# Performance work log

Measured on AMD Instinct MI355X. Metric: run time of the kernel, lower is better.

The kernel has to match this reference:

```python
import jax, jax.numpy as jnp
import numpy as np

B, S, D_MODEL, D_K, D_V, H = 2, 2048, 1024, 1024, 1024, 16


def setup_inputs() -> dict:
    key = jax.random.key(0)
    ks = jax.random.split(key, 12)
    s = 0.02
    inp = {
        "queries": jax.random.normal(ks[0], (B, S, D_MODEL), jnp.float32),
        "keys": jax.random.normal(ks[1], (B, S, D_MODEL), jnp.float32),
        "values": jax.random.normal(ks[2], (B, S, D_MODEL), jnp.float32),
        # causal mask: 1 where attention is disallowed (added as -1e9*mask)
        "mask": jnp.triu(jnp.ones((1, 1, S, S), jnp.float32), k=1),
        "Wq": jax.random.normal(ks[3], (D_MODEL, D_K), jnp.float32) * s,
        "bq": jnp.zeros((D_K,), jnp.float32),
        "Wk": jax.random.normal(ks[4], (D_MODEL, D_K), jnp.float32) * s,
        "bk": jnp.zeros((D_K,), jnp.float32),
        "Wv": jax.random.normal(ks[5], (D_MODEL, D_V), jnp.float32) * s,
        "bv": jnp.zeros((D_V,), jnp.float32),
        "Wo": jax.random.normal(ks[6], (D_K, D_MODEL), jnp.float32) * s,
        "bo": jnp.zeros((D_MODEL,), jnp.float32),
    }
    return inp


def _split_heads(x):  # [B,S,D] -> [B,H,S,D/H]
    b, s, d = x.shape
    return x.reshape(b, s, H, d // H).transpose(0, 2, 1, 3)


def reference(queries, keys, values, mask, Wq, bq, Wk, bk, Wv, bv, Wo, bo):
    q = _split_heads(queries @ Wq + bq)   # [B,H,S,hd]
    k = _split_heads(keys @ Wk + bk)
    v = _split_heads(values @ Wv + bv)
    # NOTE: original scales by sqrt(full d_k), not per-head dim (faithful quirk)
    scores = jnp.einsum("bhqd,bhkd->bhqk", q, k) / jnp.sqrt(jnp.float32(D_K))
    scores = scores + (-1e9) * mask
    w = jax.nn.softmax(scores, axis=-1)
    out = jnp.einsum("bhqk,bhkd->bhqd", w, v)        # [B,H,S,hd]
    out = out.transpose(0, 2, 1, 3).reshape(q.shape[0], q.shape[2], D_K)
    return out @ Wo + bo
```

## Files before the change

### kernel.cpp

```cpp
#include <hip/hip_runtime.h>
#include <hip/hip_bf16.h>
#include <cstdint>

typedef __bf16 bf16;
typedef __bf16 bf16x2 __attribute__((ext_vector_type(2)));
typedef __bf16 bf16x4 __attribute__((ext_vector_type(4)));
typedef __bf16 bf16x8 __attribute__((ext_vector_type(8)));
typedef float f32x4 __attribute__((ext_vector_type(4)));
typedef float f32x16 __attribute__((ext_vector_type(16)));
typedef unsigned int u32;

#define B_ 2
#define S_ 2048
#define DM 1024
#define H_ 16
#define HD 64

__device__ __forceinline__ void gload_lds16(const bf16* g, bf16* l) {
  __builtin_amdgcn_global_load_lds((const __attribute__((address_space(1))) void*)g,
                                   (__attribute__((address_space(3))) void*)l,
                                   16, 0, 0);
}

__device__ __forceinline__ u32 cvt_pk_bf16(float lo, float hi) {
  u32 r;
  asm("v_cvt_pk_bf16_f32 %0, %1, %2" : "=v"(r) : "v"(lo), "v"(hi));
  return r;
}

__global__ __launch_bounds__(256) void convert_k(const float* __restrict__ s0,
                                                 const float* __restrict__ s1,
                                                 const float* __restrict__ s2,
                                                 bf16* __restrict__ d0,
                                                 bf16* __restrict__ d1,
                                                 bf16* __restrict__ d2) {
  const float* s = (blockIdx.z == 0) ? s0 : (blockIdx.z == 1) ? s1 : s2;
  bf16* d = (blockIdx.z == 0) ? d0 : (blockIdx.z == 1) ? d1 : d2;
  const size_t i = ((size_t)blockIdx.x * 256 + threadIdx.x) * 8;
  f32x4 a = *(const f32x4*)(s + i);
  f32x4 b = *(const f32x4*)(s + i + 4);
  bf16x8 o;
#pragma unroll
  for (int j = 0; j < 4; j++) { o[j] = (bf16)a[j]; o[j + 4] = (bf16)b[j]; }
  *(bf16x8*)(d + i) = o;
}

__global__ __launch_bounds__(256) void transposeW_k(
    const float* __restrict__ w0, const float* __restrict__ w1,
    const float* __restrict__ w2, const float* __restrict__ w3,
    bf16* __restrict__ t0, bf16* __restrict__ t1,
    bf16* __restrict__ t2, bf16* __restrict__ t3) {
  const float* src = (blockIdx.z == 0) ? w0 : (blockIdx.z == 1) ? w1
                     : (blockIdx.z == 2) ? w2 : w3;
  bf16* dst = (blockIdx.z == 0) ? t0 : (blockIdx.z == 1) ? t1
              : (blockIdx.z == 2) ? t2 : t3;
  __shared__ float tile[32][33];
  const int tx = threadIdx.x, ty = threadIdx.y;
  const int x0 = blockIdx.x * 32, y0 = blockIdx.y * 32;
#pragma unroll
  for (int r = 0; r < 4; r++)
    tile[ty + r * 8][tx] = src[(size_t)(y0 + ty + r * 8) * DM + x0 + tx];
  __syncthreads();
#pragma unroll
  for (int r = 0; r < 4; r++)
    dst[(size_t)(x0 + ty + r * 8) * DM + y0 + tx] = (bf16)tile[tx][ty + r * 8];
}

struct GArgs { const void* A; const bf16* Bt; const float* bias; void* C; };
struct GArgs3 { GArgs g[3]; };

template <bool AF32, bool CF32>
__global__ __launch_bounds__(256) void gemm_k(GArgs3 args, int M, int N, int K) {
  const GArgs ga = args.g[blockIdx.z];
  __shared__ __align__(16) bf16 As[128 * 32];
  __shared__ __align__(16) bf16 Bs[128 * 32];
  const int tid = threadIdx.x;
  const int lane = tid & 63, w = tid >> 6;
  const int l15 = lane & 15, q = lane >> 4;
  const int wr = w >> 1, wc = w & 1;
  const int m0 = blockIdx.y * 128, n0 = blockIdx.x * 128;

  const int c0 = w * 128 + lane;
  const int c1 = c0 + 64;
  const int r0 = c0 >> 2, r1 = c1 >> 2, koff = (c0 & 3) * 8;
  const bf16* gB0 = ga.Bt + (size_t)(n0 + r0) * K + koff;
  const bf16* gB1 = ga.Bt + (size_t)(n0 + r1) * K + koff;
  bf16* lA0 = As + (w * 2 + 0) * 512;
  bf16* lA1 = As + (w * 2 + 1) * 512;
  bf16* lB0 = Bs + (w * 2 + 0) * 512;
  bf16* lB1 = Bs + (w * 2 + 1) * 512;

  const float* pA0 = nullptr;
  const float* pA1 = nullptr;
  f32x4 t00, t01, t10, t11;
  if constexpr (AF32) {
    const float* A = (const float*)ga.A;
    pA0 = A + (size_t)(m0 + r0) * K + koff;
    pA1 = A + (size_t)(m0 + r1) * K + koff;
    t00 = *(const f32x4*)pA0; t01 = *(const f32x4*)(pA0 + 4);
    t10 = *(const f32x4*)pA1; t11 = *(const f32x4*)(pA1 + 4);
  }

  f32x4 acc[4][4] = {};

  for (int k0 = 0; k0 < K; k0 += 32) {
    if constexpr (AF32) {
      bf16x8 va0, va1;
#pragma unroll
      for (int j = 0; j < 4; j++) {
        va0[j] = (bf16)t00[j]; va0[j + 4] = (bf16)t01[j];
        va1[j] = (bf16)t10[j]; va1[j + 4] = (bf16)t11[j];
      }
      *(bf16x8*)(lA0 + lane * 8) = va0;
      *(bf16x8*)(lA1 + lane * 8) = va1;
    } else {
      const bf16* A = (const bf16*)ga.A;
      gload_lds16(A + (size_t)(m0 + r0) * K + koff + k0, lA0);
      gload_lds16(A + (size_t)(m0 + r1) * K + koff + k0, lA1);
    }
    gload_lds16(gB0 + k0, lB0);
    gload_lds16(gB1 + k0, lB1);
    __syncthreads();

    bf16x8 a[4], b[4];
#pragma unroll
    for (int mt = 0; mt < 4; mt++)
      a[mt] = *(const bf16x8*)(As + (wr * 64 + mt * 16 + l15) * 32 + q * 8);
#pragma unroll
    for (int nt = 0; nt < 4; nt++)
      b[nt] = *(const bf16x8*)(Bs + (wc * 64 + nt * 16 + l15) * 32 + q * 8);

    if constexpr (AF32) {
      const int kn = (k0 + 32 < K) ? k0 + 32 : k0;
      t00 = *(const f32x4*)(pA0 + kn); t01 = *(const f32x4*)(pA0 + kn + 4);
      t10 = *(const f32x4*)(pA1 + kn); t11 = *(const f32x4*)(pA1 + kn + 4);
    }

#pragma unroll
    for (int mt = 0; mt < 4; mt++)
#pragma unroll
      for (int nt = 0; nt < 4; nt++)
        acc[mt][nt] = __builtin_amdgcn_mfma_f32_16x16x32_bf16(a[mt], b[nt],
                                                              acc[mt][nt], 0, 0, 0);
    __syncthreads();
  }

#pragma unroll
  for (int nt = 0; nt < 4; nt++) {
    const int col = n0 + wc * 64 + nt * 16 + l15;
    const float bv = ga.bias[col];
#pragma unroll
    for (int mt = 0; mt < 4; mt++) {
      const int row = m0 + wr * 64 + mt * 16 + q * 4;
#pragma unroll
      for (int r = 0; r < 4; r++) {
        const float val = acc[mt][nt][r] + bv;
        if constexpr (CF32)
          ((float*)ga.C)[(size_t)(row + r) * N + col] = val;
        else
          ((bf16*)ga.C)[(size_t)(row + r) * N + col] = (bf16)val;
      }
    }
  }
}

__global__ __launch_bounds__(256, 4) void attn_k(const bf16* __restrict__ Qp,
                                                 const bf16* __restrict__ Kp,
                                                 const bf16* __restrict__ Vp,
                                                 bf16* __restrict__ Op) {
  const int g = blockIdx.x;
  const int c = g & 255, sl = g >> 8;
  const int u = c & 31;
  const int xt = (sl == 0) ? u : (sl == 1) ? 31 - u
                 : (sl == 2) ? (u ^ 16) : 31 - (u ^ 16);
  const int h = (c >> 5) | ((sl & 1) << 3);
  const int b = sl >> 1;
  const int i0 = xt * 64;

  const int tid = threadIdx.x;
  const int lane = tid & 63, w = tid >> 6;
  const int l31 = lane & 31, hi = lane >> 5;
  const int qh = w >> 1, kh = w & 1;

  __shared__ __align__(16) char smem[36864];
  bf16 (*Ks)[64][72] = (bf16 (*)[64][72])smem;
  bf16 (*Vts)[64][72] = (bf16 (*)[64][72])(smem + 18432);

  const size_t headoff = (size_t)b * S_ * DM + h * HD;
  const bf16* Kb = Kp + headoff;
  const bf16* Vb = Vp + headoff;

  const int kr0 = tid >> 3, kr1 = 32 + (tid >> 3), kcb = (tid & 7) * 8;
  const int d0 = (tid & 31) * 2, kq = (tid >> 5) * 8;
  const float QSCALE = 0.04508422f;

  bf16x8 qreg[4];
  {
    const bf16* qb = Qp + headoff + (size_t)(i0 + qh * 32 + l31) * DM + hi * 8;
#pragma unroll
    for (int kk = 0; kk < 4; kk++) {
      bf16x8 v = *(const bf16x8*)(qb + kk * 16);
      bf16x8 o;
#pragma unroll
      for (int j = 0; j < 8; j++) o[j] = (bf16)((float)v[j] * QSCALE);
      qreg[kk] = o;
    }
  }

  {
    bf16x8 k0v = *(const bf16x8*)(Kb + (size_t)kr0 * DM + kcb);
    bf16x8 k1v = *(const bf16x8*)(Kb + (size_t)kr1 * DM + kcb);
    *(bf16x8*)&Ks[0][kr0][kcb] = k0v;
    *(bf16x8*)&Ks[0][kr1][kcb] = k1v;
    bf16x8 vlo, vhi;
#pragma unroll
    for (int j = 0; j < 8; j++) {
      bf16x2 p = *(const bf16x2*)(Vb + (size_t)(kq + j) * DM + d0);
      vlo[j] = p[0]; vhi[j] = p[1];
    }
    *(bf16x8*)&Vts[0][d0][kq] = vlo;
    *(bf16x8*)&Vts[0][d0 + 1][kq] = vhi;
  }
  __syncthreads();

  f32x16 oacc0 = {}, oacc1 = {};
  float rsum = 0.f;
  int buf = 0;

  for (int j0 = 0; j0 <= i0; j0 += 64, buf ^= 1) {
    const int jn = (j0 + 64 <= i0) ? j0 + 64 : 0;
    bf16x8 kpre0 = *(const bf16x8*)(Kb + (size_t)(jn + kr0) * DM + kcb);
    bf16x8 kpre1 = *(const bf16x8*)(Kb + (size_t)(jn + kr1) * DM + kcb);
    bf16x2 vpre[8];
#pragma unroll
    for (int j = 0; j < 8; j++)
      vpre[j] = *(const bf16x2*)(Vb + (size_t)(jn + kq + j) * DM + d0);

    const bool diag = (j0 == i0);
    if (!(diag && kh > qh)) {
      f32x16 sacc = {};
      __builtin_amdgcn_s_setprio(1);
#pragma unroll
      for (int kk = 0; kk < 4; kk++) {
        bf16x8 ka = *(const bf16x8*)&Ks[buf][kh * 32 + l31][kk * 16 + hi * 8];
        sacc = __builtin_amdgcn_mfma_f32_32x32x16_bf16(ka, qreg[kk], sacc, 0, 0, 0);
      }
      __builtin_amdgcn_s_setprio(0);

      float p[16];
      if (diag) {
        const int qrl = qh * 32 + l31;
#pragma unroll
        for (int r = 0; r < 16; r++) {
          const int keyl = kh * 32 + (r & 3) + 8 * (r >> 2) + 4 * hi;
          p[r] = (keyl <= qrl) ? __builtin_amdgcn_exp2f(sacc[r]) : 0.f;
          rsum += p[r];
        }
      } else {
#pragma unroll
        for (int r = 0; r < 16; r++) {
          p[r] = __builtin_amdgcn_exp2f(sacc[r]);
          rsum += p[r];
        }
      }

      u32 Aq[4][2];
#pragma unroll
      for (int t = 0; t < 4; t++) {
        Aq[t][0] = cvt_pk_bf16(p[4 * t + 0], p[4 * t + 1]);
        Aq[t][1] = cvt_pk_bf16(p[4 * t + 2], p[4 * t + 3]);
      }
      bf16x8 pb[2];
#pragma unroll
      for (int s = 0; s < 2; s++) {
        auto e0 = __builtin_amdgcn_permlane32_swap(Aq[2 * s][0], Aq[2 * s + 1][0], false, false);
        auto e1 = __builtin_amdgcn_permlane32_swap(Aq[2 * s][1], Aq[2 * s + 1][1], false, false);
        union { u32 u[4]; bf16x8 v; } cv;
        cv.u[0] = e0[0]; cv.u[1] = e1[0]; cv.u[2] = e0[1]; cv.u[3] = e1[1];
        pb[s] = cv.v;
      }

      __builtin_amdgcn_s_setprio(1);
#pragma unroll
      for (int s = 0; s < 2; s++) {
        bf16x8 va0 = *(const bf16x8*)&Vts[buf][l31][kh * 32 + s * 16 + hi * 8];
        bf16x8 va1 = *(const bf16x8*)&Vts[buf][32 + l31][kh * 32 + s * 16 + hi * 8];
        oacc0 = __builtin_amdgcn_mfma_f32_32x32x16_bf16(va0, pb[s], oacc0, 0, 0, 0);
        oacc1 = __builtin_amdgcn_mfma_f32_32x32x16_bf16(va1, pb[s], oacc1, 0, 0, 0);
      }
      __builtin_amdgcn_s_setprio(0);
    }

    *(bf16x8*)&Ks[buf ^ 1][kr0][kcb] = kpre0;
    *(bf16x8*)&Ks[buf ^ 1][kr1][kcb] = kpre1;
    {
      bf16x8 vlo, vhi;
#pragma unroll
      for (int j = 0; j < 8; j++) { vlo[j] = vpre[j][0]; vhi[j] = vpre[j][1]; }
      *(bf16x8*)&Vts[buf ^ 1][d0][kq] = vlo;
      *(bf16x8*)&Vts[buf ^ 1][d0 + 1][kq] = vhi;
    }
    __syncthreads();
  }

  float rtot_w = rsum + __shfl_xor(rsum, 32);
  float* osum = (float*)smem;
  float* auxf = (float*)(smem + 32768);
#pragma unroll
  for (int m = 0; m < 2; m++) {
#pragma unroll
    for (int rq = 0; rq < 4; rq++) {
      f32x4 v4;
#pragma unroll
      for (int e = 0; e < 4; e++)
        v4[e] = m ? oacc1[rq * 4 + e] : oacc0[rq * 4 + e];
      *(f32x4*)(osum + w * 2048 + (m * 4 + rq) * 256 + lane * 4) = v4;
    }
  }
  if (lane < 32) auxf[w * 32 + lane] = rtot_w;
  __syncthreads();

  {
    const int q = tid >> 2, q31b = q & 31, qh2 = q >> 5;
    const float rtot = auxf[(qh2 * 2 + 0) * 32 + q31b] + auxf[(qh2 * 2 + 1) * 32 + q31b];
    const float rinv = 1.0f / rtot;
    const int dbase = (tid & 3) * 16;
    bf16* orow = Op + headoff + (size_t)(i0 + q) * DM + dbase;
#pragma unroll
    for (int gg = 0; gg < 2; gg++) {
      bf16x8 o8;
#pragma unroll
      for (int e = 0; e < 8; e++) {
        const int d = dbase + gg * 8 + e;
        const int base = (((d >> 5) << 2) | ((d >> 3) & 3)) * 256 +
                         (q31b + 32 * ((d >> 2) & 1)) * 4 + (d & 3);
        const float v = osum[(qh2 * 2 + 0) * 2048 + base] +
                        osum[(qh2 * 2 + 1) * 2048 + base];
        o8[e] = (bf16)(v * rinv);
      }
      *(bf16x8*)(orow + gg * 8) = o8;
    }
  }
}

extern "C" void kernel_launch(void* const* d_in, const int* in_sizes, int n_in,
                              void* d_out, int out_size, void* d_ws, size_t ws_size,
                              hipStream_t stream) {
  const float* q_in = (const float*)d_in[0];
  const float* k_in = (const float*)d_in[1];
  const float* v_in = (const float*)d_in[2];
  const float* Wq = (const float*)d_in[4];
  const float* bq = (const float*)d_in[5];
  const float* Wk = (const float*)d_in[6];
  const float* bk = (const float*)d_in[7];
  const float* Wv = (const float*)d_in[8];
  const float* bv = (const float*)d_in[9];
  const float* Wo = (const float*)d_in[10];
  const float* bo = (const float*)d_in[11];

  bf16* ws = (bf16*)d_ws;
  const size_t NQ = (size_t)B_ * S_ * DM;
  bf16* Qp = ws;
  bf16* Kp = ws + NQ;
  bf16* Vp = ws + 2 * NQ;
  bf16* WqT = ws + 3 * NQ;
  bf16* WkT = WqT + (size_t)DM * DM;
  bf16* WvT = WkT + (size_t)DM * DM;
  bf16* WoT = WvT + (size_t)DM * DM;
  bf16* qb = WoT + (size_t)DM * DM;
  bf16* kb = qb + NQ;
  bf16* vb = kb + NQ;

  const bool fast = ws_size >= (size_t)(28 * 1024 * 1024) * 2;

  transposeW_k<<<dim3(32, 32, 4), dim3(32, 8), 0, stream>>>(
      Wq, Wk, Wv, Wo, WqT, WkT, WvT, WoT);

  if (fast) {
    convert_k<<<dim3((B_ * S_ * DM) / (256 * 8), 1, 3), 256, 0, stream>>>(
        q_in, k_in, v_in, qb, kb, vb);
    GArgs3 g3;
    g3.g[0] = {qb, WqT, bq, Qp};
    g3.g[1] = {kb, WkT, bk, Kp};
    g3.g[2] = {vb, WvT, bv, Vp};
    gemm_k<false, false><<<dim3(DM / 128, (B_ * S_) / 128, 3), 256, 0, stream>>>(
        g3, B_ * S_, DM, DM);
  } else {
    GArgs3 g3;
    g3.g[0] = {q_in, WqT, bq, Qp};
    g3.g[1] = {k_in, WkT, bk, Kp};
    g3.g[2] = {v_in, WvT, bv, Vp};
    gemm_k<true, false><<<dim3(DM / 128, (B_ * S_) / 128, 3), 256, 0, stream>>>(
        g3, B_ * S_, DM, DM);
  }

  attn_k<<<dim3(1024, 1, 1), 256, 0, stream>>>(Qp, Kp, Vp, Qp);

  GArgs3 gp;
  gp.g[0] = {Qp, WoT, bo, d_out};
  gp.g[1] = gp.g[0];
  gp.g[2] = gp.g[0];
  gemm_k<false, true><<<dim3(DM / 128, (B_ * S_) / 128, 1), 256, 0, stream>>>(
      gp, B_ * S_, DM, DM);
}
```

Measured before the change: 239.0 us.

## Use 256x256-tile double-buffered GEMM with XCD remapping for QKV projection

Adds a new 512-thread GEMM kernel with 256x256 output tiles, a K-step of 64, double-buffered LDS filled by direct global-to-LDS loads, an XOR-swizzled LDS layout, and s_setprio around the MFMA blocks. The fused QKV projection now uses it with 192 workgroups, remapped so consecutive tiles land on the same XCD. The output-projection GEMM gets the same XCD-aware block remap. The goal is higher MFMA utilization and operand reuse with fewer, larger tiles. The cost is that 192 workgroups may not fill all CUs, register pressure is high, and the epilogue writes scalar bf16 stores.

```diff
diff --git a/kernel.cpp b/kernel.cpp
--- a/kernel.cpp
+++ b/kernel.cpp
@@ -69,6 +69,159 @@
 struct GArgs { const void* A; const bf16* Bt; const float* bias; void* C; };
 struct GArgs3 { GArgs g[3]; };
 
+__global__ __launch_bounds__(512, 2) void gemm256_k(GArgs3 args, int M, int N,
+                                                    int K, int tilesY, int tilesX) {
+  const int nwg = gridDim.x;
+  const int id = blockIdx.x;
+  const int wgid = (id & 7) * (nwg >> 3) + (id >> 3);
+  const int perz = tilesY * tilesX;
+  const int z = wgid / perz;
+  const int rem = wgid - z * perz;
+  const int ty = rem / tilesX, tx = rem - (rem / tilesX) * tilesX;
+  const GArgs ga = args.g[z];
+  const int m0 = ty * 256, n0 = tx * 256;
+
+  __shared__ __align__(16) bf16 As[2][16384];
+  __shared__ __align__(16) bf16 Bs[2][16384];
+
+  const int tid = threadIdx.x;
+  const int lane = tid & 63, w = tid >> 6;
+  const int l15 = lane & 15, q = lane >> 4;
+  const int wr = w >> 2, wc = w & 3;
+
+  const bf16* gA[4];
+  const bf16* gB[4];
+#pragma unroll
+  for (int i = 0; i < 4; i++) {
+    const int ci = i * 512 + w * 64 + lane;
+    const int row = ci >> 3, ch = ci & 7, sc = ch ^ (row & 7);
+    gA[i] = (const bf16*)ga.A + (size_t)(m0 + row) * K + sc * 8;
+    gB[i] = ga.Bt + (size_t)(n0 + row) * K + sc * 8;
+  }
+
+  const int cA0 = ((q) ^ (l15 & 7)) * 8;
+  const int cA1 = ((4 + q) ^ (l15 & 7)) * 8;
+
+  f32x4 acc[8][4] = {};
+
+#pragma unroll
+  for (int i = 0; i < 4; i++) {
+    gload_lds16(gA[i], &As[0][(i * 512 + w * 64) * 8]);
+    gload_lds16(gB[i], &Bs[0][(i * 512 + w * 64) * 8]);
+  }
+  asm volatile("s_waitcnt vmcnt(0)" ::: "memory");
+  __builtin_amdgcn_s_barrier();
+
+  const int NT = K >> 6;
+  for (int t = 0; t < NT; ++t) {
+    const int cur = t & 1;
+    const bf16* Ac = As[cur];
+    const bf16* Bc = Bs[cur];
+
+    bf16x8 a[4][2], b[2][2][2];
+#pragma unroll
+    for (int mt = 0; mt < 4; mt++) {
+      const int row = wr * 128 + mt * 16 + l15;
+      a[mt][0] = *(const bf16x8*)(Ac + row * 64 + cA0);
+      a[mt][1] = *(const bf16x8*)(Ac + row * 64 + cA1);
+    }
+#pragma unroll
+    for (int nt = 0; nt < 2; nt++) {
+      const int row = wc * 64 + nt * 16 + l15;
+      b[0][nt][0] = *(const bf16x8*)(Bc + row * 64 + cA0);
+      b[0][nt][1] = *(const bf16x8*)(Bc + row * 64 + cA1);
+    }
+    if (t + 1 < NT) {
+      const int k0 = (t + 1) << 6;
+      bf16* An = As[cur ^ 1];
+      bf16* Bn = Bs[cur ^ 1];
+#pragma unroll
+      for (int i = 0; i < 4; i++) {
+        gload_lds16(gA[i] + k0, An + (i * 512 + w * 64) * 8);
+        gload_lds16(gB[i] + k0, Bn + (i * 512 + w * 64) * 8);
+      }
+    }
+    __builtin_amdgcn_s_setprio(1);
+#pragma unroll
+    for (int mt = 0; mt < 4; mt++)
+#pragma unroll
+      for (int nt = 0; nt < 2; nt++)
+#pragma unroll
+        for (int kk = 0; kk < 2; kk++)
+          acc[mt][nt] = __builtin_amdgcn_mfma_f32_16x16x32_bf16(
+              a[mt][kk], b[0][nt][kk], acc[mt][nt], 0, 0, 0);
+    __builtin_amdgcn_s_setprio(0);
+    __builtin_amdgcn_s_barrier();
+
+#pragma unroll
+    for (int nt = 0; nt < 2; nt++) {
+      const int row = wc * 64 + 32 + nt * 16 + l15;
+      b[1][nt][0] = *(const bf16x8*)(Bc + row * 64 + cA0);
+      b[1][nt][1] = *(const bf16x8*)(Bc + row * 64 + cA1);
+    }
+    __builtin_amdgcn_s_setprio(1);
+#pragma unroll
+    for (int mt = 0; mt < 4; mt++)
+#pragma unroll
+      for (int nt = 0; nt < 2; nt++)
+#pragma unroll
+        for (int kk = 0; kk < 2; kk++)
+          acc[mt][2 + nt] = __builtin_amdgcn_mfma_f32_16x16x32_bf16(
+              a[mt][kk], b[1][nt][kk], acc[mt][2 + nt], 0, 0, 0);
+    __builtin_amdgcn_s_setprio(0);
+    __builtin_amdgcn_s_barrier();
+
+#pragma unroll
+    for (int mt = 0; mt < 4; mt++) {
+      const int row = wr * 128 + 64 + mt * 16 + l15;
+      a[mt][0] = *(const bf16x8*)(Ac + row * 64 + cA0);
+      a[mt][1] = *(const bf16x8*)(Ac + row * 64 + cA1);
+    }
+    __builtin_amdgcn_s_setprio(1);
+#pragma unroll
+    for (int mt = 0; mt < 4; mt++)
+#pragma unroll
+      for (int nt = 0; nt < 2; nt++)
+#pragma unroll
+        for (int kk = 0; kk < 2; kk++)
+          acc[4 + mt][2 + nt] = __builtin_amdgcn_mfma_f32_16x16x32_bf16(
+              a[mt][kk], b[1][nt][kk], acc[4 + mt][2 + nt], 0, 0, 0);
+    __builtin_amdgcn_s_setprio(0);
+    __builtin_amdgcn_s_barrier();
+
+    __builtin_amdgcn_s_setprio(1);
+#pragma unroll
+    for (int mt = 0; mt < 4; mt++)
+#pragma unroll
+      for (int nt = 0; nt < 2; nt++)
+#pragma unroll
+        for (int kk = 0; kk < 2; kk++)
+          acc[4 + mt][nt] = __builtin_amdgcn_mfma_f32_16x16x32_bf16(
+              a[mt][kk], b[0][nt][kk], acc[4 + mt][nt], 0, 0, 0);
+    __builtin_amdgcn_s_setprio(0);
+    asm volatile("s_waitcnt vmcnt(0)" ::: "memory");
+    __builtin_amdgcn_s_barrier();
+  }
+
+#pragma unroll
+  for (int nh = 0; nh < 2; nh++)
+#pragma unroll
+    for (int nt = 0; nt < 2; nt++) {
+      const int col = n0 + wc * 64 + nh * 32 + nt * 16 + l15;
+      const float bv = ga.bias[col];
+#pragma unroll
+      for (int mh = 0; mh < 2; mh++)
+#pragma unroll
+        for (int mt = 0; mt < 4; mt++) {
+          const int row = m0 + wr * 128 + mh * 64 + mt * 16 + q * 4;
+          f32x4 v = acc[mh * 4 + mt][nh * 2 + nt];
+#pragma unroll
+          for (int r = 0; r < 4; r++)
+            ((bf16*)ga.C)[(size_t)(row + r) * N + col] = (bf16)(v[r] + bv);
+        }
+    }
+}
+
 template <bool AF32, bool CF32>
 __global__ __launch_bounds__(256) void gemm_k(GArgs3 args, int M, int N, int K) {
   const GArgs ga = args.g[blockIdx.z];
@@ -78,7 +231,16 @@
   const int lane = tid & 63, w = tid >> 6;
   const int l15 = lane & 15, q = lane >> 4;
   const int wr = w >> 1, wc = w & 1;
-  const int m0 = blockIdx.y * 128, n0 = blockIdx.x * 128;
+
+  int bx = blockIdx.x, by = blockIdx.y;
+  if constexpr (CF32) {
+    const int nb = gridDim.x * gridDim.y;
+    const int id = by * gridDim.x + bx;
+    const int wg = (id & 7) * (nb >> 3) + (id >> 3);
+    bx = wg % gridDim.x;
+    by = wg / gridDim.x;
+  }
+  const int m0 = by * 128, n0 = bx * 128;
 
   const int c0 = w * 128 + lane;
   const int c1 = c0 + 64;
@@ -383,8 +545,7 @@
     g3.g[0] = {qb, WqT, bq, Qp};
     g3.g[1] = {kb, WkT, bk, Kp};
     g3.g[2] = {vb, WvT, bv, Vp};
-    gemm_k<false, false><<<dim3(DM / 128, (B_ * S_) / 128, 3), 256, 0, stream>>>(
-        g3, B_ * S_, DM, DM);
+    gemm256_k<<<dim3(192), 512, 0, stream>>>(g3, B_ * S_, DM, DM, 16, 4);
   } else {
     GArgs3 g3;
     g3.g[0] = {q_in, WqT, bq, Qp};
```

New measurement: 225.5 us. 1.06x faster.
